# Kernel tuning notes

Hardware: AMD Instinct MI355X
Metric: run time of the kernel (lower is better)

Reference implementation:

```python
import jax, jax.numpy as jnp
import numpy as np

NUM_HEADS = 16
MAX_BATCH = 4
MAX_SEQ = 2048


def setup_inputs() -> dict:
    key = jax.random.key(0)
    ks = jax.random.split(key, 9)
    B, S, H = 4, 2048, 2048
    scale = 0.02
    hidden_state = jax.random.normal(ks[0], (B, S, H), dtype=jnp.float32)
    # causal mask (masked_fill where mask == 0), broadcastable over batch/heads
    mask = jnp.tril(jnp.ones((S, S), dtype=jnp.int32))[None, None]  # [1,1,S,S]
    Wq = jax.random.normal(ks[1], (H, H), dtype=jnp.float32) * scale
    Wk = jax.random.normal(ks[2], (H, H), dtype=jnp.float32) * scale
    Wv = jax.random.normal(ks[3], (H, H), dtype=jnp.float32) * scale
    Wo = jax.random.normal(ks[4], (H, H), dtype=jnp.float32) * scale
    bq = jax.random.normal(ks[5], (H,), dtype=jnp.float32) * scale
    bk = jax.random.normal(ks[6], (H,), dtype=jnp.float32) * scale
    bv = jax.random.normal(ks[7], (H,), dtype=jnp.float32) * scale
    bo = jax.random.normal(ks[8], (H,), dtype=jnp.float32) * scale
    return {"hidden_state": hidden_state, "mask": mask,
            "Wq": Wq, "bq": bq, "Wk": Wk, "bk": bk,
            "Wv": Wv, "bv": bv, "Wo": Wo, "bo": bo,
            "start_pos": 0}


def reference(hidden_state, mask, Wq, bq, Wk, bk, Wv, bv, Wo, bo, start_pos):
    B, S, H = hidden_state.shape
    nh = NUM_HEADS
    hd = H // nh
    # qkv projections (nn.Linear: x @ W.T + b)
    q = (hidden_state @ Wq.T + bq).reshape(B, S, nh, hd)
    k = (hidden_state @ Wk.T + bk).reshape(B, S, nh, hd)
    v = (hidden_state @ Wv.T + bv).reshape(B, S, nh, hd)
    # KV-cache append (zeros-initialized buffer, write [start_pos:start_pos+S])
    cache_k = jnp.zeros((MAX_BATCH, MAX_SEQ, nh, hd), dtype=q.dtype)
    cache_v = jnp.zeros((MAX_BATCH, MAX_SEQ, nh, hd), dtype=q.dtype)
    cache_k = jax.lax.dynamic_update_slice(cache_k, k, (0, start_pos, 0, 0))
    cache_v = jax.lax.dynamic_update_slice(cache_v, v, (0, start_pos, 0, 0))
    total = start_pos + S
    key = cache_k[:B, :total]   # [B, total, nh, hd]
    value = cache_v[:B, :total]
    # scores: [B, nh, S, total]
    scores = jnp.einsum('bqhd,bkhd->bhqk', q, key) / jnp.sqrt(jnp.float32(hd))
    scores = jnp.where(mask == 0, -jnp.inf, scores)
    probs = jax.nn.softmax(scores, axis=-1)
    out = jnp.einsum('bhqk,bkhd->bqhd', probs, value).reshape(B, S, H)
    return out @ Wo.T + bo
```

## Files before the change

kernel.cpp:

```cpp
#include <hip/hip_runtime.h>
#include <hip/hip_bf16.h>
#include <stdint.h>

#define S_LEN 2048
#define HDIM  2048
#define NH    16
#define HD    128
#define BATCH 4

typedef __attribute__((ext_vector_type(8))) short bf16x8;
typedef __attribute__((ext_vector_type(4))) float f32x4;
typedef __attribute__((ext_vector_type(4))) float float4v;
typedef __attribute__((ext_vector_type(4))) unsigned short u16x4;

__device__ __forceinline__ void gload_lds16(const void* g, void* l) {
  __builtin_amdgcn_global_load_lds(
      (const __attribute__((address_space(1))) unsigned int*)g,
      (__attribute__((address_space(3))) unsigned int*)l,
      16, 0, 0);
}

__device__ __forceinline__ unsigned short f2bf(float x) {
  __hip_bfloat16 b = __float2bfloat16(x);
  return *reinterpret_cast<unsigned short*>(&b);
}

#define SL2E 0.1275174465f

__global__ __launch_bounds__(256) void cvt_kernel(const float* __restrict__ in,
                                                  unsigned short* __restrict__ out,
                                                  int n4) {
  int stride = gridDim.x * blockDim.x;
  for (int i = blockIdx.x * blockDim.x + threadIdx.x; i < n4; i += stride) {
    float4v v = *(const float4v*)(in + (size_t)i * 4);
    u16x4 o;
    o.x = f2bf(v.x); o.y = f2bf(v.y); o.z = f2bf(v.z); o.w = f2bf(v.w);
    *(u16x4*)(out + (size_t)i * 4) = o;
  }
}

__global__ __launch_bounds__(256) void cvt4_kernel(
    const float* __restrict__ w0, const float* __restrict__ w1,
    const float* __restrict__ w2, const float* __restrict__ w3,
    unsigned short* __restrict__ o0, unsigned short* __restrict__ o1,
    unsigned short* __restrict__ o2, unsigned short* __restrict__ o3,
    int n4) {
  const int y = blockIdx.y;
  const float* in = (y == 0) ? w0 : (y == 1) ? w1 : (y == 2) ? w2 : w3;
  unsigned short* out = (y == 0) ? o0 : (y == 1) ? o1 : (y == 2) ? o2 : o3;
  int stride = gridDim.x * blockDim.x;
  for (int i = blockIdx.x * blockDim.x + threadIdx.x; i < n4; i += stride) {
    float4v v = *(const float4v*)(in + (size_t)i * 4);
    u16x4 o;
    o.x = f2bf(v.x); o.y = f2bf(v.y); o.z = f2bf(v.z); o.w = f2bf(v.w);
    *(u16x4*)(out + (size_t)i * 4) = o;
  }
}


#define G8_VMW(N) asm volatile("s_waitcnt vmcnt(" #N ")" ::: "memory")
#define G8_BAR1() do { __builtin_amdgcn_sched_barrier(0); __builtin_amdgcn_s_barrier(); \
  asm volatile("s_waitcnt lgkmcnt(0)" ::: "memory"); __builtin_amdgcn_sched_barrier(0); } while (0)
#define G8_BAR2() do { __builtin_amdgcn_sched_barrier(0); __builtin_amdgcn_s_barrier(); \
  __builtin_amdgcn_sched_barrier(0); } while (0)

#define G8_STAGE(ISB, BUF, HALF, KT) do {                                          \
  int kt_ = (KT); if (kt_ > nkt1) kt_ = nkt1;                                      \
  const char* gs_ = ((ISB) ? Bg : Ag) +                                            \
      (size_t)(((ISB) ? bn : bm) * 256 + (HALF) * 128 + w * 16) * (size_t)K2 +     \
      (size_t)kt_ * 128;                                                           \
  char* ld_ = lds + (BUF) * 65536 + (ISB) * 32768 + ((HALF) * 128 + w * 16) * 128; \
  gload_lds16(gs_ + sLn, ld_);                                                     \
  gload_lds16(gs_ + 8 * (size_t)K2 + sLn, ld_ + 1024);                             \
} while (0)

#define G8_RDA(BUF, MI0) do {                                                      \
  _Pragma("unroll") for (int mi = 0; mi < 4; ++mi)                                 \
  _Pragma("unroll") for (int kk = 0; kk < 2; ++kk)                                 \
    a[mi][kk] = *(const bf16x8*)(lds + (BUF) * 65536 +                             \
        (wm + ((MI0) + mi) * 16 + ln) * 128 + ((((kk << 2) + g) ^ ln7) << 4));     \
} while (0)

#define G8_RDB(BUF, NI0, BREG) do {                                                \
  _Pragma("unroll") for (int ni = 0; ni < 2; ++ni)                                 \
  _Pragma("unroll") for (int kk = 0; kk < 2; ++kk)                                 \
    BREG[ni][kk] = *(const bf16x8*)(lds + (BUF) * 65536 + 32768 +                  \
        (wn + ((NI0) + ni) * 16 + ln) * 128 + ((((kk << 2) + g) ^ ln7) << 4));     \
} while (0)

#define G8_MFMA(M0, N0, BREG) do {                                                 \
  __builtin_amdgcn_s_setprio(1);                                                   \
  _Pragma("unroll") for (int mi = 0; mi < 4; ++mi)                                 \
  _Pragma("unroll") for (int ni = 0; ni < 2; ++ni)                                 \
  _Pragma("unroll") for (int kk = 0; kk < 2; ++kk)                                 \
    acc[(M0) + mi][(N0) + ni] = __builtin_amdgcn_mfma_f32_16x16x32_bf16(           \
        a[mi][kk], BREG[ni][kk], acc[(M0) + mi][(N0) + ni], 0, 0, 0);              \
  __builtin_amdgcn_s_setprio(0);                                                   \
} while (0)

template<int OUTMODE>
__global__ __launch_bounds__(512, 2) void gemm8(
    const __hip_bfloat16* __restrict__ A, const __hip_bfloat16* __restrict__ B,
    const float* __restrict__ bias, void* __restrict__ C,
    int M, int N, int K, float scale) {
  __shared__ char lds[131072];
  const int tid = threadIdx.x;
  const int w = tid >> 6;
  const int lane = tid & 63;
  const int g = lane >> 4;
  const int ln = lane & 15;
  const int ln7 = lane & 7;
  const int K2 = K * 2;
  const int nkt = K >> 6;
  const int nkt1 = nkt - 1;
  const int niter = nkt >> 1;

  const int NBN = N >> 8;
  const int nwg = (M >> 8) * NBN;
  const int cpx = nwg >> 3;
  const int bid = blockIdx.x;
  const int wg = (bid & 7) * cpx + (bid >> 3);
  const int bm = wg / NBN, bn = wg % NBN;

  const int wm = (w >> 2) * 128;
  const int wn = (w & 3) * 64;

  const char* Ag = (const char*)A;
  const char* Bg = (const char*)B;
  const size_t sLn = (size_t)(lane >> 3) * (size_t)K2 +
                     (size_t)(((lane & 7) ^ (lane >> 3)) << 4);

  f32x4 acc[8][4];
#pragma unroll
  for (int mi = 0; mi < 8; ++mi)
#pragma unroll
    for (int ni = 0; ni < 4; ++ni) acc[mi][ni] = (f32x4){0.f, 0.f, 0.f, 0.f};

  G8_STAGE(0, 0, 0, 0); G8_STAGE(0, 0, 1, 0);
  G8_STAGE(1, 0, 0, 0); G8_STAGE(1, 0, 1, 0);
  G8_STAGE(1, 1, 0, 1); G8_STAGE(1, 1, 1, 1);
  G8_VMW(4);
  G8_BAR2();

  for (int i = 0; i < niter; ++i) {
    const int v = 2 * i + 1, u2 = 2 * i + 2, v2 = 2 * i + 3;
    bf16x8 a[4][2], b0[2][2], b1[2][2];
    G8_RDA(0, 0); G8_RDB(0, 0, b0);
    G8_STAGE(0, 1, 0, v);
    G8_BAR1();
    G8_MFMA(0, 0, b0);
    G8_BAR2();
    G8_RDB(0, 2, b1);
    G8_STAGE(0, 1, 1, v);
    G8_BAR1();
    G8_MFMA(0, 2, b1);
    G8_BAR2();
    G8_RDA(0, 4);
    G8_STAGE(1, 0, 0, u2);
    G8_BAR1();
    G8_MFMA(4, 0, b0);
    G8_BAR2();
    G8_STAGE(1, 0, 1, u2);
    G8_VMW(4);
    G8_BAR1();
    G8_MFMA(4, 2, b1);
    G8_BAR2();
    G8_RDA(1, 0); G8_RDB(1, 0, b0);
    G8_STAGE(0, 0, 0, u2);
    G8_BAR1();
    G8_MFMA(0, 0, b0);
    G8_BAR2();
    G8_RDB(1, 2, b1);
    G8_STAGE(0, 0, 1, u2);
    G8_BAR1();
    G8_MFMA(0, 2, b1);
    G8_BAR2();
    G8_RDA(1, 4);
    G8_STAGE(1, 1, 0, v2);
    G8_BAR1();
    G8_MFMA(4, 0, b0);
    G8_BAR2();
    G8_STAGE(1, 1, 1, v2);
    G8_VMW(4);
    G8_BAR1();
    G8_MFMA(4, 2, b1);
    G8_BAR2();
  }

  G8_VMW(0);
#pragma unroll
  for (int ni = 0; ni < 4; ++ni) {
    const int col = bn * 256 + wn + ni * 16 + ln;
    const float bv = bias[col];
#pragma unroll
    for (int mi = 0; mi < 8; ++mi) {
      const int row0 = bm * 256 + wm + mi * 16 + g * 4;
      if (OUTMODE == 2) {
        const int h = col >> 7, d = col & 127;
        const size_t base = ((size_t)((row0 >> 11) * NH + h) * HD + d) * S_LEN +
                            (row0 & (S_LEN - 1));
        u16x4 pk;
#pragma unroll
        for (int r = 0; r < 4; ++r)
          pk[r] = f2bf((acc[mi][ni][r] + bv) * scale);
        *(u16x4*)((unsigned short*)C + base) = pk;
      } else {
#pragma unroll
        for (int r = 0; r < 4; ++r) {
          float val = (acc[mi][ni][r] + bv) * scale;
          if (OUTMODE == 1)
            ((float*)C)[(size_t)(row0 + r) * N + col] = val;
          else
            ((__hip_bfloat16*)C)[(size_t)(row0 + r) * N + col] = __float2bfloat16(val);
        }
      }
    }
  }
}

#define DEFER_THR 8.0f

__global__ __launch_bounds__(256, 2) void attn_kernel(
    const __hip_bfloat16* __restrict__ Q, const __hip_bfloat16* __restrict__ Kg,
    const __hip_bfloat16* __restrict__ Vt, __hip_bfloat16* __restrict__ O) {
  __shared__ char lds[49152];
  const int tid = threadIdx.x;
  const int w = tid >> 6;
  const int lane = tid & 63;
  const int g = lane >> 4;
  const int ln = lane & 15;
  const int bh = blockIdx.y;
  const int b = bh >> 4, h = bh & 15;

  const char* Qb = (const char*)Q + ((size_t)b * S_LEN * HDIM + h * HD) * 2;
  const char* Kb = (const char*)Kg + ((size_t)b * S_LEN * HDIM + h * HD) * 2;
  const char* Vb = (const char*)Vt + ((size_t)bh * HD * S_LEN) * 2;
  char* ldsK = lds;
  char* ldsV = lds + 16384;
  char* pw   = lds + 32768 + w * 4096;

  const int kr = lane >> 4;
  const int kc = lane & 15;
  const int vr = lane >> 3;
  const int vc = lane & 7;

  auto stage = [&](int kv0) {
#pragma unroll
    for (int i = 0; i < 4; i++) {
      int r = w * 16 + i * 4 + kr;
      gload_lds16(Kb + (size_t)(kv0 + r) * (HDIM * 2) + ((kc ^ (r & 7)) << 4),
                  ldsK + (w * 16 + i * 4) * 256);
    }
#pragma unroll
    for (int i = 0; i < 4; i++) {
      int r = w * 32 + i * 8 + vr;
      gload_lds16(Vb + (size_t)r * (S_LEN * 2) + (size_t)kv0 * 2 + ((vc ^ vr) << 4),
                  ldsV + (w * 32 + i * 8) * 128);
    }
  };

  for (int pass = 0; pass < 2; pass++) {
    const int qt = pass == 0 ? (15 - (int)blockIdx.x) : (int)blockIdx.x;
    const int q0 = qt * 128 + w * 32;

    const int nt = 2 * qt + 2;
    __syncthreads();
    stage(0);

    bf16x8 qf[2][4];
#pragma unroll
    for (int qs = 0; qs < 2; qs++)
#pragma unroll
      for (int dc = 0; dc < 4; dc++)
        qf[qs][dc] = *(const bf16x8*)(Qb + (size_t)(q0 + qs * 16 + ln) * HDIM * 2 +
                                      (dc * 32 + g * 8) * 2);

    f32x4 o[2][8];
#pragma unroll
    for (int qs = 0; qs < 2; qs++)
#pragma unroll
      for (int ds = 0; ds < 8; ds++) o[qs][ds] = (f32x4){0.f, 0.f, 0.f, 0.f};
    float mrun[2][4], lrun[2][4];
#pragma unroll
    for (int qs = 0; qs < 2; qs++)
#pragma unroll
      for (int r = 0; r < 4; r++) { mrun[qs][r] = -__builtin_inff(); lrun[qs][r] = 0.f; }

    __syncthreads();

    for (int t = 0; t < nt; t++) {
      const int kv0 = t * 64;

      if (kv0 <= q0 + 31) {
        f32x4 sa[2][4];
#pragma unroll
        for (int qs = 0; qs < 2; qs++)
#pragma unroll
          for (int ks = 0; ks < 4; ks++) sa[qs][ks] = (f32x4){0.f, 0.f, 0.f, 0.f};
#pragma unroll
        for (int dc = 0; dc < 4; dc++) {
          bf16x8 kf[4];
#pragma unroll
          for (int ks = 0; ks < 4; ks++)
            kf[ks] = *(const bf16x8*)(ldsK + (ks * 16 + ln) * 256 +
                                      (((dc * 4 + g) ^ (ln & 7)) << 4));
#pragma unroll
          for (int qs = 0; qs < 2; qs++)
#pragma unroll
            for (int ks = 0; ks < 4; ks++)
              sa[qs][ks] = __builtin_amdgcn_mfma_f32_16x16x32_bf16(qf[qs][dc], kf[ks], sa[qs][ks], 0, 0, 0);
        }
        const bool needmask = (kv0 + 63) > q0;
        if (needmask) {
#pragma unroll
          for (int qs = 0; qs < 2; qs++)
#pragma unroll
            for (int ks = 0; ks < 4; ks++)
#pragma unroll
              for (int r = 0; r < 4; r++)
                if ((kv0 + ks * 16 + ln) > (q0 + qs * 16 + g * 4 + r))
                  sa[qs][ks][r] = -__builtin_inff();
        }
        float pmax[2][4];
#pragma unroll
        for (int qs = 0; qs < 2; qs++)
#pragma unroll
          for (int r = 0; r < 4; r++) {
            float mx = fmaxf(fmaxf(sa[qs][0][r], sa[qs][1][r]), fmaxf(sa[qs][2][r], sa[qs][3][r]));
            mx = fmaxf(mx, __shfl_xor(mx, 1));
            mx = fmaxf(mx, __shfl_xor(mx, 2));
            mx = fmaxf(mx, __shfl_xor(mx, 4));
            mx = fmaxf(mx, __shfl_xor(mx, 8));
            pmax[qs][r] = mx;
          }
        float dmin = 1e30f;
#pragma unroll
        for (int qs = 0; qs < 2; qs++)
#pragma unroll
          for (int r = 0; r < 4; r++)
            dmin = fminf(dmin, mrun[qs][r] + DEFER_THR - pmax[qs][r]);
        if (!__all(dmin >= 0.0f)) {
          float alpha[2][4];
#pragma unroll
          for (int qs = 0; qs < 2; qs++)
#pragma unroll
            for (int r = 0; r < 4; r++) {
              float mn = fmaxf(mrun[qs][r], pmax[qs][r]);
              alpha[qs][r] = exp2f(mrun[qs][r] - mn);
              mrun[qs][r] = mn;
              lrun[qs][r] *= alpha[qs][r];
            }
#pragma unroll
          for (int qs = 0; qs < 2; qs++)
#pragma unroll
            for (int ds = 0; ds < 8; ds++)
#pragma unroll
              for (int r = 0; r < 4; r++) o[qs][ds][r] *= alpha[qs][r];
        }
        float rsum[2][4];
#pragma unroll
        for (int qs = 0; qs < 2; qs++)
#pragma unroll
          for (int r = 0; r < 4; r++) rsum[qs][r] = 0.f;
#pragma unroll
        for (int qs = 0; qs < 2; qs++)
#pragma unroll
          for (int ks = 0; ks < 4; ks++)
#pragma unroll
            for (int r = 0; r < 4; r++) {
              float p = exp2f(sa[qs][ks][r] - mrun[qs][r]);
              sa[qs][ks][r] = p;
              rsum[qs][r] += p;
            }
#pragma unroll
        for (int qs = 0; qs < 2; qs++)
#pragma unroll
          for (int r = 0; r < 4; r++) {
            float rs = rsum[qs][r];
            rs += __shfl_xor(rs, 1);
            rs += __shfl_xor(rs, 2);
            rs += __shfl_xor(rs, 4);
            rs += __shfl_xor(rs, 8);
            lrun[qs][r] += rs;
          }
#pragma unroll
        for (int qs = 0; qs < 2; qs++)
#pragma unroll
          for (int ks = 0; ks < 4; ks++)
#pragma unroll
            for (int r = 0; r < 4; r++) {
              int row = qs * 16 + g * 4 + r;
              int key = ks * 16 + ln;
              *(__hip_bfloat16*)(pw + row * 128 + (((key >> 3) ^ (row & 7)) << 4) + (key & 7) * 2) =
                  __float2bfloat16(sa[qs][ks][r]);
            }
#pragma unroll
        for (int kk = 0; kk < 2; kk++) {
          bf16x8 pa[2];
#pragma unroll
          for (int qs = 0; qs < 2; qs++) {
            int row = qs * 16 + ln;
            pa[qs] = *(const bf16x8*)(pw + row * 128 + (((kk * 4 + g) ^ (row & 7)) << 4));
          }
#pragma unroll
          for (int ds = 0; ds < 8; ds++) {
            bf16x8 vf = *(const bf16x8*)(ldsV + (ds * 16 + ln) * 128 +
                                         (((kk * 4 + g) ^ (ln & 7)) << 4));
#pragma unroll
            for (int qs = 0; qs < 2; qs++)
              o[qs][ds] = __builtin_amdgcn_mfma_f32_16x16x32_bf16(pa[qs], vf, o[qs][ds], 0, 0, 0);
          }
        }
      }

      if (t + 1 < nt) {
        __syncthreads();
        stage(kv0 + 64);
        __syncthreads();
      }
    }
    float inv[2][4];
#pragma unroll
    for (int qs = 0; qs < 2; qs++)
#pragma unroll
      for (int r = 0; r < 4; r++) inv[qs][r] = 1.0f / lrun[qs][r];
    __hip_bfloat16* Ob = O + (size_t)b * S_LEN * HDIM + h * HD;
#pragma unroll
    for (int qs = 0; qs < 2; qs++)
#pragma unroll
      for (int ds = 0; ds < 8; ds++)
#pragma unroll
        for (int r = 0; r < 4; r++)
          Ob[(size_t)(q0 + qs * 16 + g * 4 + r) * HDIM + ds * 16 + ln] =
              __float2bfloat16(o[qs][ds][r] * inv[qs][r]);
  }
}

extern "C" void kernel_launch(void* const* d_in, const int* in_sizes, int n_in,
                              void* d_out, int out_size, void* d_ws, size_t ws_size,
                              hipStream_t stream) {
  const float* X  = (const float*)d_in[0];
  const float* Wq = (const float*)d_in[2];
  const float* bq = (const float*)d_in[3];
  const float* Wk = (const float*)d_in[4];
  const float* bk = (const float*)d_in[5];
  const float* Wv = (const float*)d_in[6];
  const float* bv = (const float*)d_in[7];
  const float* Wo = (const float*)d_in[8];
  const float* bo = (const float*)d_in[9];

  char* ws = (char*)d_ws;
  __hip_bfloat16* Xb   = (__hip_bfloat16*)(ws);
  __hip_bfloat16* Wqb  = (__hip_bfloat16*)(ws + 33554432);
  __hip_bfloat16* Wkb  = (__hip_bfloat16*)(ws + 41943040);
  __hip_bfloat16* Wvb  = (__hip_bfloat16*)(ws + 50331648);
  __hip_bfloat16* Wob  = (__hip_bfloat16*)(ws + 58720256);
  __hip_bfloat16* Qb   = (__hip_bfloat16*)(ws + 67108864);
  __hip_bfloat16* Kb   = (__hip_bfloat16*)(ws + 100663296);
  __hip_bfloat16* Ob   = (__hip_bfloat16*)(ws + 134217728);
  __hip_bfloat16* Vtb  = (__hip_bfloat16*)(ws + 167772160);

  cvt_kernel<<<2048, 256, 0, stream>>>(X,  (unsigned short*)Xb,  16777216 / 4);
  cvt4_kernel<<<dim3(512, 4), 256, 0, stream>>>(
      Wq, Wk, Wv, Wo,
      (unsigned short*)Wqb, (unsigned short*)Wkb,
      (unsigned short*)Wvb, (unsigned short*)Wob, 4194304 / 4);

  gemm8<0><<<256, 512, 0, stream>>>(Xb, Wqb, bq, Qb,  8192, 2048, 2048, SL2E);
  gemm8<0><<<256, 512, 0, stream>>>(Xb, Wkb, bk, Kb,  8192, 2048, 2048, 1.0f);
  gemm8<2><<<256, 512, 0, stream>>>(Xb, Wvb, bv, Vtb, 8192, 2048, 2048, 1.0f);

  attn_kernel<<<dim3(8, 64), 256, 0, stream>>>(Qb, Kb, Vtb, Ob);

  gemm8<1><<<256, 512, 0, stream>>>(Ob, Wob, bo, (float*)d_out, 8192, 2048, 2048, 1.0f);
}
```

Measured before the change: 450.9 us.

## Merge input conversions into one launch, reorder attention grid, add MFMA priority

Folds the X conversion and the four weight conversions into a single five-row launch, saving one kernel launch. The attention grid is transposed so consecutive blocks cover different batch-heads for the same query-tile pair, which changes dispatch order and cache locality of K/V. s_setprio raises wave priority around the MFMA loops to favour matrix-core issue. The merged X conversion row gets only 512 blocks of grid-stride work, so that row may become the tail of the conversion launch.

```diff
diff --git a/kernel.cpp b/kernel.cpp
--- a/kernel.cpp
+++ b/kernel.cpp
@@ -27,27 +27,18 @@
 
 #define SL2E 0.1275174465f
 
-__global__ __launch_bounds__(256) void cvt_kernel(const float* __restrict__ in,
-                                                  unsigned short* __restrict__ out,
-                                                  int n4) {
-  int stride = gridDim.x * blockDim.x;
-  for (int i = blockIdx.x * blockDim.x + threadIdx.x; i < n4; i += stride) {
-    float4v v = *(const float4v*)(in + (size_t)i * 4);
-    u16x4 o;
-    o.x = f2bf(v.x); o.y = f2bf(v.y); o.z = f2bf(v.z); o.w = f2bf(v.w);
-    *(u16x4*)(out + (size_t)i * 4) = o;
-  }
-}
-
-__global__ __launch_bounds__(256) void cvt4_kernel(
+__global__ __launch_bounds__(256) void cvt5_kernel(
+    const float* __restrict__ x,
     const float* __restrict__ w0, const float* __restrict__ w1,
     const float* __restrict__ w2, const float* __restrict__ w3,
+    unsigned short* __restrict__ ox,
     unsigned short* __restrict__ o0, unsigned short* __restrict__ o1,
     unsigned short* __restrict__ o2, unsigned short* __restrict__ o3,
-    int n4) {
+    int n4x, int n4w) {
   const int y = blockIdx.y;
-  const float* in = (y == 0) ? w0 : (y == 1) ? w1 : (y == 2) ? w2 : w3;
-  unsigned short* out = (y == 0) ? o0 : (y == 1) ? o1 : (y == 2) ? o2 : o3;
+  const float* in = (y == 0) ? x : (y == 1) ? w0 : (y == 2) ? w1 : (y == 3) ? w2 : w3;
+  unsigned short* out = (y == 0) ? ox : (y == 1) ? o0 : (y == 2) ? o1 : (y == 3) ? o2 : o3;
+  const int n4 = (y == 0) ? n4x : n4w;
   int stride = gridDim.x * blockDim.x;
   for (int i = blockIdx.x * blockDim.x + threadIdx.x; i < n4; i += stride) {
     float4v v = *(const float4v*)(in + (size_t)i * 4);
@@ -229,7 +220,8 @@
   const int lane = tid & 63;
   const int g = lane >> 4;
   const int ln = lane & 15;
-  const int bh = blockIdx.y;
+  const int bh = blockIdx.x;
+  const int pairid = blockIdx.y;
   const int b = bh >> 4, h = bh & 15;
 
   const char* Qb = (const char*)Q + ((size_t)b * S_LEN * HDIM + h * HD) * 2;
@@ -260,7 +252,7 @@
   };
 
   for (int pass = 0; pass < 2; pass++) {
-    const int qt = pass == 0 ? (15 - (int)blockIdx.x) : (int)blockIdx.x;
+    const int qt = pass == 0 ? (15 - pairid) : pairid;
     const int q0 = qt * 128 + w * 32;
 
     const int nt = 2 * qt + 2;
@@ -304,11 +296,13 @@
           for (int ks = 0; ks < 4; ks++)
             kf[ks] = *(const bf16x8*)(ldsK + (ks * 16 + ln) * 256 +
                                       (((dc * 4 + g) ^ (ln & 7)) << 4));
+          __builtin_amdgcn_s_setprio(1);
 #pragma unroll
           for (int qs = 0; qs < 2; qs++)
 #pragma unroll
             for (int ks = 0; ks < 4; ks++)
               sa[qs][ks] = __builtin_amdgcn_mfma_f32_16x16x32_bf16(qf[qs][dc], kf[ks], sa[qs][ks], 0, 0, 0);
+          __builtin_amdgcn_s_setprio(0);
         }
         const bool needmask = (kv0 + 63) > q0;
         if (needmask) {
@@ -402,6 +396,7 @@
             int row = qs * 16 + ln;
             pa[qs] = *(const bf16x8*)(pw + row * 128 + (((kk * 4 + g) ^ (row & 7)) << 4));
           }
+          __builtin_amdgcn_s_setprio(1);
 #pragma unroll
           for (int ds = 0; ds < 8; ds++) {
             bf16x8 vf = *(const bf16x8*)(ldsV + (ds * 16 + ln) * 128 +
@@ -410,6 +405,7 @@
             for (int qs = 0; qs < 2; qs++)
               o[qs][ds] = __builtin_amdgcn_mfma_f32_16x16x32_bf16(pa[qs], vf, o[qs][ds], 0, 0, 0);
           }
+          __builtin_amdgcn_s_setprio(0);
         }
       }
 
@@ -460,17 +456,18 @@
   __hip_bfloat16* Ob   = (__hip_bfloat16*)(ws + 134217728);
   __hip_bfloat16* Vtb  = (__hip_bfloat16*)(ws + 167772160);
 
-  cvt_kernel<<<2048, 256, 0, stream>>>(X,  (unsigned short*)Xb,  16777216 / 4);
-  cvt4_kernel<<<dim3(512, 4), 256, 0, stream>>>(
-      Wq, Wk, Wv, Wo,
+  cvt5_kernel<<<dim3(512, 5), 256, 0, stream>>>(
+      X, Wq, Wk, Wv, Wo,
+      (unsigned short*)Xb,
       (unsigned short*)Wqb, (unsigned short*)Wkb,
-      (unsigned short*)Wvb, (unsigned short*)Wob, 4194304 / 4);
+      (unsigned short*)Wvb, (unsigned short*)Wob,
+      16777216 / 4, 4194304 / 4);
 
   gemm8<0><<<256, 512, 0, stream>>>(Xb, Wqb, bq, Qb,  8192, 2048, 2048, SL2E);
   gemm8<0><<<256, 512, 0, stream>>>(Xb, Wkb, bk, Kb,  8192, 2048, 2048, 1.0f);
   gemm8<2><<<256, 512, 0, stream>>>(Xb, Wvb, bv, Vtb, 8192, 2048, 2048, 1.0f);
 
-  attn_kernel<<<dim3(8, 64), 256, 0, stream>>>(Qb, Kb, Vtb, Ob);
+  attn_kernel<<<dim3(64, 8), 256, 0, stream>>>(Qb, Kb, Vtb, Ob);
 
   gemm8<1><<<256, 512, 0, stream>>>(Ob, Wob, bo, (float*)d_out, 8192, 2048, 2048, 1.0f);
 }
```

New measurement: 433.9 us. 3.8% less time.
